# Optimization experiments

Hardware: AMD Instinct MI355X
Metric: run time of the kernel (lower is better)

The kernel has to match this reference:

```python
import jax, jax.numpy as jnp
import numpy as np

B, N, C = 2048, 64, 384
H, WS, HIDDEN, TEMB = 12, 8, 64, 384
D = C // H


def _rpb_index(ws):
    coords = np.stack(np.meshgrid(np.arange(ws), np.arange(ws), indexing='ij'))  # (2, ws, ws)
    flat = coords.reshape(2, -1)                       # (2, ws*ws)
    rel = flat[:, :, None] - flat[:, None, :]          # (2, N, N)
    rel = rel.transpose(1, 2, 0).copy()                # (N, N, 2)
    rel[..., 0] += ws - 1
    rel[..., 1] += ws - 1
    rel[..., 0] *= 2 * ws - 1
    return rel.sum(-1)                                  # (N, N) int


def setup_inputs() -> dict:
    key = jax.random.key(0)
    ks = jax.random.split(key, 16)
    s = 0.02
    inp = {
        'x': jax.random.normal(ks[0], (B, N, C), jnp.float32),
        'temb': jax.random.normal(ks[1], (B, TEMB), jnp.float32),
        'sigma': jax.random.uniform(ks[2], (B,), jnp.float32, 1e-3, 1.0),
        'qkv_w': jax.random.normal(ks[3], (C, 3 * C), jnp.float32) * s,
        'qkv_b': jax.random.normal(ks[4], (3 * C,), jnp.float32) * s,
        'qkvt_w': jax.random.normal(ks[5], (TEMB, 3 * C), jnp.float32) * s,
        'trunk_w1': jax.random.normal(ks[6], (1, HIDDEN), jnp.float32) * s,
        'trunk_b1': jax.random.normal(ks[7], (HIDDEN,), jnp.float32) * s,
        'trunk_w2': jax.random.normal(ks[8], (HIDDEN, HIDDEN), jnp.float32) * s,
        'trunk_b2': jax.random.normal(ks[9], (HIDDEN,), jnp.float32) * s,
        'gate_w': jax.random.normal(ks[10], (HIDDEN, 1), jnp.float32) * s,
        'gate_b': jnp.zeros((1,), jnp.float32),
        'bias_w': jax.random.normal(ks[11], (HIDDEN, H), jnp.float32) * s,
        'bias_b': jax.random.normal(ks[12], (H,), jnp.float32) * s,
        'proj_w': jax.random.normal(ks[13], (C, C), jnp.float32) * s,
        'proj_b': jax.random.normal(ks[14], (C,), jnp.float32) * s,
        'rpb_table': jax.random.normal(ks[15], ((2 * WS - 1) * (2 * WS - 1), H), jnp.float32) * s,
        'rpb_index': jnp.asarray(_rpb_index(WS), jnp.int32),
    }
    return inp


def reference(x, temb, sigma, qkv_w, qkv_b, qkvt_w, trunk_w1, trunk_b1,
              trunk_w2, trunk_b2, gate_w, gate_b, bias_w, bias_b,
              proj_w, proj_b, rpb_table, rpb_index):
    b, n, c = x.shape
    h, d = H, c // H
    scale = d ** -0.5
    # QKV with time-embedding modulation
    qkv = x @ qkv_w + qkv_b + (temb @ qkvt_w)[:, None, :]        # (B, N, 3C)
    qkv = qkv.reshape(b, n, 3, h, d).transpose(2, 0, 3, 1, 4)     # (3, B, H, N, D)
    q, k, v = qkv[0], qkv[1], qkv[2]
    attn = jnp.einsum('bhnd,bhmd->bhnm', q * scale, k)            # (B, H, N, N)
    # relative position bias
    rpb = rpb_table[rpb_index].transpose(2, 0, 1)                 # (H, N, N)
    attn = attn + rpb[None]
    # noise-conditioned gate and per-head bias
    log_sigma = jnp.log(jnp.clip(sigma, 1e-6))[:, None]           # (B, 1)
    hid = jax.nn.silu(log_sigma @ trunk_w1 + trunk_b1)
    hid = jax.nn.silu(hid @ trunk_w2 + trunk_b2)                  # (B, hidden)
    gate = jax.nn.sigmoid(hid @ gate_w + gate_b).reshape(b, 1, 1, 1)
    nbias = (hid @ bias_w + bias_b).reshape(b, h, 1, 1)
    attn = attn / (1.0 + gate) + nbias
    attn = jax.nn.softmax(attn, axis=-1)
    out = jnp.einsum('bhnm,bhmd->bhnd', attn, v)                  # (B, H, N, D)
    out = out.transpose(0, 2, 1, 3).reshape(b, n, c)
    return out @ proj_w + proj_b
```

## Files before the change

kernel.cpp:

```cpp
#include <hip/hip_runtime.h>

#define B_TOT 2048
#define SEQ 64
#define CH 384
#define NH 12
#define HD 32
#define NC3 1152
#define LDP 392
#define QKS 40
#define VS 72
#define HDSZ 7424
#define QK_SCALE 0.17677669529663687f

typedef __attribute__((ext_vector_type(8))) short short8;
typedef __attribute__((ext_vector_type(4))) short short4v;
typedef __attribute__((ext_vector_type(4))) float f32x4;
typedef unsigned short u16;

__device__ __forceinline__ u16 f2bf(float f) {
  unsigned int u = __float_as_uint(f);
  u += 0x7fffu + ((u >> 16) & 1u);
  return (u16)(u >> 16);
}
__device__ __forceinline__ float bf2f(u16 u) {
  return __uint_as_float(((unsigned int)u) << 16);
}

__device__ __forceinline__ int pswz(int row, int col) {
  return row * 64 + ((((col >> 3) ^ (row & 7)) << 3) | (col & 7));
}

__global__ void k_prep(const float* __restrict__ qkv_w, const float* __restrict__ proj_w,
                       const float* __restrict__ rpb_table, const int* __restrict__ rpb_index,
                       u16* __restrict__ qkvwt, u16* __restrict__ projwt, u16* __restrict__ rpbz)
{
  int idx = blockIdx.x * 256 + threadIdx.x;
  if (idx < CH * NC3) {
    int k = idx / NC3, n = idx - k * NC3;
    qkvwt[n * LDP + k] = f2bf(qkv_w[idx]);
    return;
  }
  idx -= CH * NC3;
  if (idx < CH * CH) {
    int k = idx / CH, n = idx - k * CH;
    projwt[n * LDP + k] = f2bf(proj_w[idx]);
    return;
  }
  idx -= CH * CH;
  if (idx < NH * SEQ * SEQ) {
    int h = idx >> 12, j = (idx >> 6) & 63, q = idx & 63;
    int jt = j >> 4, g4j = (j >> 2) & 3, r = j & 3;
    int qt = q >> 4, q16 = q & 15;
    int dst = (h * 16 + jt * 4 + qt) * 256 + g4j * 64 + q16 * 4 + r;
    rpbz[dst] = f2bf(rpb_table[rpb_index[q * 64 + j] * NH + h]);
  }
}

__global__ void k_trunk(const float* __restrict__ sigma, const float* __restrict__ w1,
                        const float* __restrict__ b1, const float* __restrict__ w2,
                        const float* __restrict__ b2, const float* __restrict__ gw,
                        const float* __restrict__ gb, const float* __restrict__ bw,
                        const float* __restrict__ bb,
                        float* __restrict__ inv1pg, float* __restrict__ nbias)
{
  int b = blockIdx.x, j = threadIdx.x;
  __shared__ float sh[64];
  float ls = logf(fmaxf(sigma[b], 1e-6f));
  float z = fmaf(ls, w1[j], b1[j]);
  z = z / (1.f + __expf(-z));
  sh[j] = z;
  __syncthreads();
  float a = b2[j];
  #pragma unroll 8
  for (int i = 0; i < 64; ++i) a = fmaf(sh[i], w2[i * 64 + j], a);
  a = a / (1.f + __expf(-a));
  __syncthreads();
  sh[j] = a;
  __syncthreads();
  if (j == 0) {
    float zg = gb[0];
    #pragma unroll 8
    for (int i = 0; i < 64; ++i) zg = fmaf(sh[i], gw[i], zg);
    float gate = 1.f / (1.f + __expf(-zg));
    inv1pg[b] = 1.f / (1.f + gate);
  }
  if (j < NH) {
    float zb = bb[j];
    #pragma unroll 8
    for (int i = 0; i < 64; ++i) zb = fmaf(sh[i], bw[i * NH + j], zb);
    nbias[b * NH + j] = zb;
  }
}

__global__ __launch_bounds__(256) void k_tvec(const float* __restrict__ temb,
                                              const float* __restrict__ qkvt_w,
                                              const float* __restrict__ qkv_b,
                                              float* __restrict__ tvec)
{
  __shared__ float st[16 * 384];
  int bi = blockIdx.x;
  int brow = bi / 9, cseg = bi - brow * 9;
  int cb = cseg * 128;
  int tid = threadIdx.x;
  for (int idx = tid; idx < 16 * 384; idx += 256) {
    int r = idx / 384, k = idx - r * 384;
    st[idx] = temb[(brow * 16 + r) * 384 + k];
  }
  __syncthreads();
  int cl = tid & 127, half = tid >> 7;
  float acc[8];
  #pragma unroll
  for (int i = 0; i < 8; ++i) acc[i] = 0.f;
  #pragma unroll 4
  for (int k = 0; k < 384; ++k) {
    float w = qkvt_w[k * NC3 + cb + cl];
    #pragma unroll
    for (int i = 0; i < 8; ++i) acc[i] = fmaf(st[(half * 8 + i) * 384 + k], w, acc[i]);
  }
  float qb = qkv_b[cb + cl];
  #pragma unroll
  for (int i = 0; i < 8; ++i)
    tvec[(brow * 16 + half * 8 + i) * NC3 + cb + cl] = acc[i] + qb;
}

template<int NT>
__device__ __forceinline__ void qkv_tiles(const u16* __restrict__ sx, u16* __restrict__ shd,
                                          const u16* __restrict__ qkvwt,
                                          const float* __restrict__ tvb,
                                          int g, int nt0, int q16, int g4)
{
  const f32x4 fz = {0.f, 0.f, 0.f, 0.f};
  float tv[NT][2]; const u16* bp[NT]; int mh6[NT], hj6[NT], hf6[NT];
  #pragma unroll
  for (int i = 0; i < NT; ++i) {
    int nt = nt0 + i;
    int hj = nt / 6, wi = nt - hj * 6;
    int mh = wi >> 1, hf = wi & 1;
    mh6[i] = mh; hj6[i] = hj; hf6[i] = hf;
    int c = mh * CH + (g * 2 + hj) * HD + hf * 16 + q16;
    tv[i][0] = tvb[c];
    tv[i][1] = tvb[NC3 + c];
    bp[i] = qkvwt + c * LDP + g4 * 8;
  }
  f32x4 acc[8][NT];
  #pragma unroll
  for (int m = 0; m < 8; ++m)
    #pragma unroll
    for (int i = 0; i < NT; ++i) acc[m][i] = fz;
  #pragma unroll 2
  for (int kt = 0; kt < 12; ++kt) {
    short8 af[8];
    #pragma unroll
    for (int m = 0; m < 8; ++m)
      af[m] = *reinterpret_cast<const short8*>(&sx[(m * 16 + q16) * LDP + kt * 32 + g4 * 8]);
    #pragma unroll
    for (int i = 0; i < NT; ++i) {
      short8 bf = *reinterpret_cast<const short8*>(bp[i] + kt * 32);
      #pragma unroll
      for (int m = 0; m < 8; ++m)
        acc[m][i] = __builtin_amdgcn_mfma_f32_16x16x32_bf16(af[m], bf, acc[m][i], 0, 0, 0);
    }
  }
  #pragma unroll
  for (int i = 0; i < NT; ++i) {
    int cof = hf6[i] * 16 + q16;
    #pragma unroll
    for (int m = 0; m < 8; ++m) {
      int bt = m >> 2;
      u16* hbase = &shd[(bt * 2 + hj6[i]) * HDSZ];
      int mrow = (m & 3) * 16 + g4 * 4;
      f32x4 a = acc[m][i];
      float tvv = tv[i][bt];
      if (mh6[i] == 0) {
        #pragma unroll
        for (int r = 0; r < 4; ++r)
          hbase[(mrow + r) * QKS + cof] = f2bf((a[r] + tvv) * QK_SCALE);
      } else if (mh6[i] == 1) {
        #pragma unroll
        for (int r = 0; r < 4; ++r)
          hbase[2560 + (mrow + r) * QKS + cof] = f2bf(a[r] + tvv);
      } else {
        short4v pk;
        #pragma unroll
        for (int r = 0; r < 4; ++r) pk[r] = (short)f2bf(a[r] + tvv);
        *reinterpret_cast<short4v*>(&hbase[5120 + cof * VS + mrow]) = pk;
      }
    }
  }
}

__global__ __launch_bounds__(512, 2) void k_attn(
    const float* __restrict__ x, const float* __restrict__ tvec,
    const float* __restrict__ inv1pg, const float* __restrict__ nbias,
    const u16* __restrict__ qkvwt, const u16* __restrict__ rpbz,
    u16* __restrict__ attw)
{
  __shared__ __align__(16) u16 s_x[128 * LDP];
  __shared__ __align__(16) u16 s_hd[4 * HDSZ];
  const f32x4 fz = {0.f, 0.f, 0.f, 0.f};

  const int b0 = blockIdx.x * 2;
  const int tid = threadIdx.x;
  const int w = tid >> 6, l = tid & 63;
  const int q16 = l & 15, g4 = l >> 4;

  {
    const float* xb = x + (size_t)b0 * (SEQ * CH);
    #pragma unroll 4
    for (int it = 0; it < 24; ++it) {
      int fi = it * 512 + tid;
      int row = fi / 96, c4 = fi - row * 96;
      const float4 a = *reinterpret_cast<const float4*>(xb + fi * 4);
      short4v v;
      v[0] = (short)f2bf(a.x); v[1] = (short)f2bf(a.y);
      v[2] = (short)f2bf(a.z); v[3] = (short)f2bf(a.w);
      *reinterpret_cast<short4v*>(&s_x[row * LDP + c4 * 4]) = v;
    }
  }
  __syncthreads();

  const float invb0 = inv1pg[b0], invb1 = inv1pg[b0 + 1];
  const float* tvb = tvec + (size_t)b0 * NC3;

  const int nt0 = (w < 4) ? 2 * w : 8 + (w - 4);

  for (int g = 0; g < 6; ++g) {
    if (w < 4) qkv_tiles<2>(s_x, s_hd, qkvwt, tvb, g, nt0, q16, g4);
    else       qkv_tiles<1>(s_x, s_hd, qkvwt, tvb, g, nt0, q16, g4);
    __syncthreads();

    f32x4 st2[2][4];
    #pragma unroll
    for (int t = 0; t < 2; ++t) {
      const int tau = w * 2 + t;
      const int cmb = tau >> 2, qt = tau & 3;
      const int bt = cmb >> 1, hh = cmb & 1;
      const int h = g * 2 + hh;
      const u16* sq = &s_hd[cmb * HDSZ];
      const u16* sk = sq + 2560;
      const float inv = bt ? invb1 : invb0;
      const float nb = nbias[(b0 + bt) * NH + h];

      short4v rp4[4];
      #pragma unroll
      for (int jt = 0; jt < 4; ++jt)
        rp4[jt] = *reinterpret_cast<const short4v*>(
            &rpbz[(h * 16 + jt * 4 + qt) * 256 + g4 * 64 + q16 * 4]);

      short8 bq = *reinterpret_cast<const short8*>(&sq[(qt * 16 + q16) * QKS + g4 * 8]);
      #pragma unroll
      for (int jt = 0; jt < 4; ++jt) {
        short8 ak = *reinterpret_cast<const short8*>(&sk[(jt * 16 + q16) * QKS + g4 * 8]);
        st2[t][jt] = __builtin_amdgcn_mfma_f32_16x16x32_bf16(ak, bq, fz, 0, 0, 0);
      }
      float mx = -1e30f;
      #pragma unroll
      for (int jt = 0; jt < 4; ++jt)
        #pragma unroll
        for (int r = 0; r < 4; ++r) {
          float s = fmaf(st2[t][jt][r], inv, fmaf(bf2f((u16)rp4[jt][r]), inv, nb));
          st2[t][jt][r] = s;
          mx = fmaxf(mx, s);
        }
      mx = fmaxf(mx, __shfl_xor(mx, 16));
      mx = fmaxf(mx, __shfl_xor(mx, 32));
      float sum = 0.f;
      #pragma unroll
      for (int jt = 0; jt < 4; ++jt)
        #pragma unroll
        for (int r = 0; r < 4; ++r) {
          float p = __expf(st2[t][jt][r] - mx);
          st2[t][jt][r] = p;
          sum += p;
        }
      sum += __shfl_xor(sum, 16);
      sum += __shfl_xor(sum, 32);
      float rn = 1.f / sum;
      #pragma unroll
      for (int jt = 0; jt < 4; ++jt)
        #pragma unroll
        for (int r = 0; r < 4; ++r) st2[t][jt][r] *= rn;
    }
    __syncthreads();
    #pragma unroll
    for (int t = 0; t < 2; ++t) {
      const int tau = w * 2 + t;
      const int cmb = tau >> 2, qt = tau & 3;
      const int bt = cmb >> 1, hh = cmb & 1;
      const int h = g * 2 + hh;
      u16* sq = &s_hd[cmb * HDSZ];
      const u16* svt = sq + 5120;
      u16* P = sq;

      #pragma unroll
      for (int jt = 0; jt < 4; ++jt) {
        short4v pk;
        #pragma unroll
        for (int r = 0; r < 4; ++r) pk[r] = (short)f2bf(st2[t][jt][r]);
        *reinterpret_cast<short4v*>(&P[pswz(qt * 16 + q16, jt * 16 + 4 * g4)]) = pk;
      }
      f32x4 o[2];
      o[0] = fz; o[1] = fz;
      #pragma unroll
      for (int kk = 0; kk < 2; ++kk) {
        short8 ap = *reinterpret_cast<const short8*>(
            &P[pswz(qt * 16 + q16, kk * 32 + g4 * 8)]);
        #pragma unroll
        for (int dt = 0; dt < 2; ++dt) {
          short8 bv = *reinterpret_cast<const short8*>(
              &svt[(dt * 16 + q16) * VS + kk * 32 + g4 * 8]);
          o[dt] = __builtin_amdgcn_mfma_f32_16x16x32_bf16(ap, bv, o[dt], 0, 0, 0);
        }
      }
      u16* ab = attw + (size_t)(b0 + bt) * (SEQ * CH);
      #pragma unroll
      for (int dt = 0; dt < 2; ++dt)
        #pragma unroll
        for (int r = 0; r < 4; ++r)
          ab[(qt * 16 + g4 * 4 + r) * CH + h * HD + dt * 16 + q16] = f2bf(o[dt][r]);
    }
    __syncthreads();
  }
}

__global__ __launch_bounds__(512, 2) void k_proj(
    const u16* __restrict__ attw, const u16* __restrict__ projwt,
    const float* __restrict__ proj_b, float* __restrict__ out)
{
  __shared__ __align__(16) u16 s_a[128 * LDP];
  const f32x4 fz = {0.f, 0.f, 0.f, 0.f};
  const int tid = threadIdx.x;
  const int w = tid >> 6, l = tid & 63;
  const int q16 = l & 15, g4 = l >> 4;
  const size_t row0 = (size_t)blockIdx.x * 128;

  {
    const u16* ab = attw + row0 * CH;
    #pragma unroll 4
    for (int it = 0; it < 12; ++it) {
      int slot = it * 512 + tid;
      int row = slot / 48, c8 = slot - row * 48;
      short8 v = *reinterpret_cast<const short8*>(ab + row * CH + c8 * 8);
      *reinterpret_cast<short8*>(&s_a[row * LDP + c8 * 8]) = v;
    }
  }
  __syncthreads();

  const u16* bpw[3]; float4 pb4[3];
  #pragma unroll
  for (int i = 0; i < 3; ++i) {
    int nt = w * 3 + i;
    bpw[i] = projwt + (nt * 16 + q16) * LDP + g4 * 8;
    pb4[i] = *reinterpret_cast<const float4*>(&proj_b[nt * 16 + 4 * g4]);
  }
  f32x4 acc[8][3];
  #pragma unroll
  for (int m = 0; m < 8; ++m)
    #pragma unroll
    for (int i = 0; i < 3; ++i) acc[m][i] = fz;
  #pragma unroll 2
  for (int kt = 0; kt < 12; ++kt) {
    short8 af[8];
    #pragma unroll
    for (int m = 0; m < 8; ++m)
      af[m] = *reinterpret_cast<const short8*>(&s_a[(m * 16 + q16) * LDP + kt * 32 + g4 * 8]);
    #pragma unroll
    for (int i = 0; i < 3; ++i) {
      short8 bf = *reinterpret_cast<const short8*>(bpw[i] + kt * 32);
      #pragma unroll
      for (int m = 0; m < 8; ++m)
        acc[m][i] = __builtin_amdgcn_mfma_f32_16x16x32_bf16(bf, af[m], acc[m][i], 0, 0, 0);
    }
  }
  float* ob = out + row0 * CH;
  #pragma unroll
  for (int i = 0; i < 3; ++i) {
    int cb = (w * 3 + i) * 16 + 4 * g4;
    #pragma unroll
    for (int m = 0; m < 8; ++m) {
      float4 v;
      v.x = acc[m][i][0] + pb4[i].x;
      v.y = acc[m][i][1] + pb4[i].y;
      v.z = acc[m][i][2] + pb4[i].z;
      v.w = acc[m][i][3] + pb4[i].w;
      *reinterpret_cast<float4*>(&ob[(m * 16 + q16) * CH + cb]) = v;
    }
  }
}

extern "C" void kernel_launch(void* const* d_in, const int* in_sizes, int n_in,
                              void* d_out, int out_size, void* d_ws, size_t ws_size,
                              hipStream_t stream) {
  const float* x       = (const float*)d_in[0];
  const float* temb    = (const float*)d_in[1];
  const float* sigma   = (const float*)d_in[2];
  const float* qkv_w   = (const float*)d_in[3];
  const float* qkv_b   = (const float*)d_in[4];
  const float* qkvt_w  = (const float*)d_in[5];
  const float* w1      = (const float*)d_in[6];
  const float* b1      = (const float*)d_in[7];
  const float* w2      = (const float*)d_in[8];
  const float* b2      = (const float*)d_in[9];
  const float* gw      = (const float*)d_in[10];
  const float* gb      = (const float*)d_in[11];
  const float* bw      = (const float*)d_in[12];
  const float* bb      = (const float*)d_in[13];
  const float* proj_w  = (const float*)d_in[14];
  const float* proj_b  = (const float*)d_in[15];
  const float* rpb_tab = (const float*)d_in[16];
  const int*   rpb_idx = (const int*)d_in[17];
  float* out = (float*)d_out;

  char* ws = (char*)d_ws;
  float* tvec   = (float*)(ws);
  float* inv1pg = (float*)(ws + 9437184);
  float* nbias  = (float*)(ws + 9445376);
  u16*   qkvwt  = (u16*)  (ws + 9543680);
  u16*   projwt = (u16*)  (ws + 10446848);
  u16*   rpbz   = (u16*)  (ws + 10747904);
  u16*   attw   = (u16*)  (ws + 10846208);

  k_prep<<<2496, 256, 0, stream>>>(qkv_w, proj_w, rpb_tab, rpb_idx, qkvwt, projwt, rpbz);
  k_trunk<<<2048, 64, 0, stream>>>(sigma, w1, b1, w2, b2, gw, gb, bw, bb, inv1pg, nbias);
  k_tvec<<<1152, 256, 0, stream>>>(temb, qkvt_w, qkv_b, tvec);
  k_attn<<<1024, 512, 0, stream>>>(x, tvec, inv1pg, nbias, qkvwt, rpbz, attw);
  k_proj<<<1024, 512, 0, stream>>>(attw, projwt, proj_b, out);
}
```

Measured before the change: 436.6 us.

## Rebalance QKV tile split across waves, add MFMA priority, halve proj tile

The QKV projection in k_attn previously gave 4 waves two N-tiles and 4 waves one N-tile. It now gives every wave 3 N-tiles over one batch element's 64 rows, which removes that load imbalance. s_setprio is raised around the MFMA bursts in the QKV, QK^T, PV and projection loops so matrix issue is favoured over other waves. k_proj now uses 64-row tiles with twice the blocks and launch_bounds(512,4) to raise occupancy, at the cost of reloading the projection weights more often.

```diff
diff --git a/kernel.cpp b/kernel.cpp
--- a/kernel.cpp
+++ b/kernel.cpp
@@ -123,72 +123,6 @@
     tvec[(brow * 16 + half * 8 + i) * NC3 + cb + cl] = acc[i] + qb;
 }
 
-template<int NT>
-__device__ __forceinline__ void qkv_tiles(const u16* __restrict__ sx, u16* __restrict__ shd,
-                                          const u16* __restrict__ qkvwt,
-                                          const float* __restrict__ tvb,
-                                          int g, int nt0, int q16, int g4)
-{
-  const f32x4 fz = {0.f, 0.f, 0.f, 0.f};
-  float tv[NT][2]; const u16* bp[NT]; int mh6[NT], hj6[NT], hf6[NT];
-  #pragma unroll
-  for (int i = 0; i < NT; ++i) {
-    int nt = nt0 + i;
-    int hj = nt / 6, wi = nt - hj * 6;
-    int mh = wi >> 1, hf = wi & 1;
-    mh6[i] = mh; hj6[i] = hj; hf6[i] = hf;
-    int c = mh * CH + (g * 2 + hj) * HD + hf * 16 + q16;
-    tv[i][0] = tvb[c];
-    tv[i][1] = tvb[NC3 + c];
-    bp[i] = qkvwt + c * LDP + g4 * 8;
-  }
-  f32x4 acc[8][NT];
-  #pragma unroll
-  for (int m = 0; m < 8; ++m)
-    #pragma unroll
-    for (int i = 0; i < NT; ++i) acc[m][i] = fz;
-  #pragma unroll 2
-  for (int kt = 0; kt < 12; ++kt) {
-    short8 af[8];
-    #pragma unroll
-    for (int m = 0; m < 8; ++m)
-      af[m] = *reinterpret_cast<const short8*>(&sx[(m * 16 + q16) * LDP + kt * 32 + g4 * 8]);
-    #pragma unroll
-    for (int i = 0; i < NT; ++i) {
-      short8 bf = *reinterpret_cast<const short8*>(bp[i] + kt * 32);
-      #pragma unroll
-      for (int m = 0; m < 8; ++m)
-        acc[m][i] = __builtin_amdgcn_mfma_f32_16x16x32_bf16(af[m], bf, acc[m][i], 0, 0, 0);
-    }
-  }
-  #pragma unroll
-  for (int i = 0; i < NT; ++i) {
-    int cof = hf6[i] * 16 + q16;
-    #pragma unroll
-    for (int m = 0; m < 8; ++m) {
-      int bt = m >> 2;
-      u16* hbase = &shd[(bt * 2 + hj6[i]) * HDSZ];
-      int mrow = (m & 3) * 16 + g4 * 4;
-      f32x4 a = acc[m][i];
-      float tvv = tv[i][bt];
-      if (mh6[i] == 0) {
-        #pragma unroll
-        for (int r = 0; r < 4; ++r)
-          hbase[(mrow + r) * QKS + cof] = f2bf((a[r] + tvv) * QK_SCALE);
-      } else if (mh6[i] == 1) {
-        #pragma unroll
-        for (int r = 0; r < 4; ++r)
-          hbase[2560 + (mrow + r) * QKS + cof] = f2bf(a[r] + tvv);
-      } else {
-        short4v pk;
-        #pragma unroll
-        for (int r = 0; r < 4; ++r) pk[r] = (short)f2bf(a[r] + tvv);
-        *reinterpret_cast<short4v*>(&hbase[5120 + cof * VS + mrow]) = pk;
-      }
-    }
-  }
-}
-
 __global__ __launch_bounds__(512, 2) void k_attn(
     const float* __restrict__ x, const float* __restrict__ tvec,
     const float* __restrict__ inv1pg, const float* __restrict__ nbias,
@@ -222,11 +156,71 @@
   const float invb0 = inv1pg[b0], invb1 = inv1pg[b0 + 1];
   const float* tvb = tvec + (size_t)b0 * NC3;
 
-  const int nt0 = (w < 4) ? 2 * w : 8 + (w - 4);
+  const int btA = w & 1;
+  const int nset = w >> 1;
 
   for (int g = 0; g < 6; ++g) {
-    if (w < 4) qkv_tiles<2>(s_x, s_hd, qkvwt, tvb, g, nt0, q16, g4);
-    else       qkv_tiles<1>(s_x, s_hd, qkvwt, tvb, g, nt0, q16, g4);
+    {
+      float tv[3]; const u16* bp[3]; int mh6[3], hj6[3], hf6[3];
+      #pragma unroll
+      for (int i = 0; i < 3; ++i) {
+        int nt = nset * 3 + i;
+        int hj = nt / 6, wi = nt - hj * 6;
+        int mh = wi >> 1, hf = wi & 1;
+        mh6[i] = mh; hj6[i] = hj; hf6[i] = hf;
+        int c = mh * CH + (g * 2 + hj) * HD + hf * 16 + q16;
+        tv[i] = tvb[btA * NC3 + c];
+        bp[i] = qkvwt + c * LDP + g4 * 8;
+      }
+      f32x4 acc[4][3];
+      #pragma unroll
+      for (int m = 0; m < 4; ++m)
+        #pragma unroll
+        for (int i = 0; i < 3; ++i) acc[m][i] = fz;
+      #pragma unroll 2
+      for (int kt = 0; kt < 12; ++kt) {
+        short8 af[4];
+        #pragma unroll
+        for (int m = 0; m < 4; ++m)
+          af[m] = *reinterpret_cast<const short8*>(
+              &s_x[(btA * 64 + m * 16 + q16) * LDP + kt * 32 + g4 * 8]);
+        short8 bf[3];
+        #pragma unroll
+        for (int i = 0; i < 3; ++i)
+          bf[i] = *reinterpret_cast<const short8*>(bp[i] + kt * 32);
+        __builtin_amdgcn_s_setprio(1);
+        #pragma unroll
+        for (int i = 0; i < 3; ++i)
+          #pragma unroll
+          for (int m = 0; m < 4; ++m)
+            acc[m][i] = __builtin_amdgcn_mfma_f32_16x16x32_bf16(af[m], bf[i], acc[m][i], 0, 0, 0);
+        __builtin_amdgcn_s_setprio(0);
+      }
+      #pragma unroll
+      for (int i = 0; i < 3; ++i) {
+        u16* hbase = &s_hd[(btA * 2 + hj6[i]) * HDSZ];
+        int cof = hf6[i] * 16 + q16;
+        #pragma unroll
+        for (int m = 0; m < 4; ++m) {
+          int mrow = m * 16 + g4 * 4;
+          f32x4 a = acc[m][i];
+          if (mh6[i] == 0) {
+            #pragma unroll
+            for (int r = 0; r < 4; ++r)
+              hbase[(mrow + r) * QKS + cof] = f2bf((a[r] + tv[i]) * QK_SCALE);
+          } else if (mh6[i] == 1) {
+            #pragma unroll
+            for (int r = 0; r < 4; ++r)
+              hbase[2560 + (mrow + r) * QKS + cof] = f2bf(a[r] + tv[i]);
+          } else {
+            short4v pk;
+            #pragma unroll
+            for (int r = 0; r < 4; ++r) pk[r] = (short)f2bf(a[r] + tv[i]);
+            *reinterpret_cast<short4v*>(&hbase[5120 + cof * VS + mrow]) = pk;
+          }
+        }
+      }
+    }
     __syncthreads();
 
     f32x4 st2[2][4];
@@ -248,11 +242,13 @@
             &rpbz[(h * 16 + jt * 4 + qt) * 256 + g4 * 64 + q16 * 4]);
 
       short8 bq = *reinterpret_cast<const short8*>(&sq[(qt * 16 + q16) * QKS + g4 * 8]);
+      __builtin_amdgcn_s_setprio(1);
       #pragma unroll
       for (int jt = 0; jt < 4; ++jt) {
         short8 ak = *reinterpret_cast<const short8*>(&sk[(jt * 16 + q16) * QKS + g4 * 8]);
         st2[t][jt] = __builtin_amdgcn_mfma_f32_16x16x32_bf16(ak, bq, fz, 0, 0, 0);
       }
+      __builtin_amdgcn_s_setprio(0);
       float mx = -1e30f;
       #pragma unroll
       for (int jt = 0; jt < 4; ++jt)
@@ -305,12 +301,14 @@
       for (int kk = 0; kk < 2; ++kk) {
         short8 ap = *reinterpret_cast<const short8*>(
             &P[pswz(qt * 16 + q16, kk * 32 + g4 * 8)]);
+        __builtin_amdgcn_s_setprio(1);
         #pragma unroll
         for (int dt = 0; dt < 2; ++dt) {
           short8 bv = *reinterpret_cast<const short8*>(
               &svt[(dt * 16 + q16) * VS + kk * 32 + g4 * 8]);
           o[dt] = __builtin_amdgcn_mfma_f32_16x16x32_bf16(ap, bv, o[dt], 0, 0, 0);
         }
+        __builtin_amdgcn_s_setprio(0);
       }
       u16* ab = attw + (size_t)(b0 + bt) * (SEQ * CH);
       #pragma unroll
@@ -323,21 +321,21 @@
   }
 }
 
-__global__ __launch_bounds__(512, 2) void k_proj(
+__global__ __launch_bounds__(512, 4) void k_proj(
     const u16* __restrict__ attw, const u16* __restrict__ projwt,
     const float* __restrict__ proj_b, float* __restrict__ out)
 {
-  __shared__ __align__(16) u16 s_a[128 * LDP];
+  __shared__ __align__(16) u16 s_a[64 * LDP];
   const f32x4 fz = {0.f, 0.f, 0.f, 0.f};
   const int tid = threadIdx.x;
   const int w = tid >> 6, l = tid & 63;
   const int q16 = l & 15, g4 = l >> 4;
-  const size_t row0 = (size_t)blockIdx.x * 128;
+  const size_t row0 = (size_t)blockIdx.x * 64;
 
   {
     const u16* ab = attw + row0 * CH;
-    #pragma unroll 4
-    for (int it = 0; it < 12; ++it) {
+    #pragma unroll
+    for (int it = 0; it < 6; ++it) {
       int slot = it * 512 + tid;
       int row = slot / 48, c8 = slot - row * 48;
       short8 v = *reinterpret_cast<const short8*>(ab + row * CH + c8 * 8);
@@ -353,31 +351,35 @@
     bpw[i] = projwt + (nt * 16 + q16) * LDP + g4 * 8;
     pb4[i] = *reinterpret_cast<const float4*>(&proj_b[nt * 16 + 4 * g4]);
   }
-  f32x4 acc[8][3];
+  f32x4 acc[4][3];
   #pragma unroll
-  for (int m = 0; m < 8; ++m)
+  for (int m = 0; m < 4; ++m)
     #pragma unroll
     for (int i = 0; i < 3; ++i) acc[m][i] = fz;
   #pragma unroll 2
   for (int kt = 0; kt < 12; ++kt) {
-    short8 af[8];
-    #pragma unroll
-    for (int m = 0; m < 8; ++m)
+    short8 af[4];
+    #pragma unroll
+    for (int m = 0; m < 4; ++m)
       af[m] = *reinterpret_cast<const short8*>(&s_a[(m * 16 + q16) * LDP + kt * 32 + g4 * 8]);
-    #pragma unroll
-    for (int i = 0; i < 3; ++i) {
-      short8 bf = *reinterpret_cast<const short8*>(bpw[i] + kt * 32);
-      #pragma unroll
-      for (int m = 0; m < 8; ++m)
-        acc[m][i] = __builtin_amdgcn_mfma_f32_16x16x32_bf16(bf, af[m], acc[m][i], 0, 0, 0);
-    }
+    short8 bf[3];
+    #pragma unroll
+    for (int i = 0; i < 3; ++i)
+      bf[i] = *reinterpret_cast<const short8*>(bpw[i] + kt * 32);
+    __builtin_amdgcn_s_setprio(1);
+    #pragma unroll
+    for (int i = 0; i < 3; ++i)
+      #pragma unroll
+      for (int m = 0; m < 4; ++m)
+        acc[m][i] = __builtin_amdgcn_mfma_f32_16x16x32_bf16(bf[i], af[m], acc[m][i], 0, 0, 0);
+    __builtin_amdgcn_s_setprio(0);
   }
   float* ob = out + row0 * CH;
   #pragma unroll
   for (int i = 0; i < 3; ++i) {
     int cb = (w * 3 + i) * 16 + 4 * g4;
     #pragma unroll
-    for (int m = 0; m < 8; ++m) {
+    for (int m = 0; m < 4; ++m) {
       float4 v;
       v.x = acc[m][i][0] + pb4[i].x;
       v.y = acc[m][i][1] + pb4[i].y;
@@ -424,5 +426,5 @@
   k_trunk<<<2048, 64, 0, stream>>>(sigma, w1, b1, w2, b2, gw, gb, bw, bb, inv1pg, nbias);
   k_tvec<<<1152, 256, 0, stream>>>(temb, qkvt_w, qkv_b, tvec);
   k_attn<<<1024, 512, 0, stream>>>(x, tvec, inv1pg, nbias, qkvwt, rpbz, attw);
-  k_proj<<<1024, 512, 0, stream>>>(attw, projwt, proj_b, out);
-}
+  k_proj<<<2048, 512, 0, stream>>>(attw, projwt, proj_b, out);
+}
```

Result: slower. 456.9 us (+4.6%).
